# Kernel tuning notes

Measured on AMD Instinct MI355X. Metric: run time of the kernel, lower is better.

Reference implementation:

```python
import jax, jax.numpy as jnp
import numpy as np

B, SQ, QD = 8, 4096, 1280
SCTX, CD = 93, 2048
HEADS, DIM_HEAD = 20, 64
INNER = HEADS * DIM_HEAD  # 1280


def setup_inputs() -> dict:
    key = jax.random.key(0)
    ks = jax.random.split(key, 10)
    inp = {
        'x': jax.random.normal(ks[0], (B, SQ, QD), dtype=jnp.float32),
        'context': jax.random.normal(ks[1], (B, SCTX, CD), dtype=jnp.float32),
        'scale': jax.random.uniform(ks[2], (), dtype=jnp.float32),
        'num_img_token': 16,
        # learned parameters (PyTorch nn.Linear weight layout: [out, in])
        'Wq': jax.random.normal(ks[3], (INNER, QD), dtype=jnp.float32) * 0.02,
        'Wk': jax.random.normal(ks[4], (INNER, CD), dtype=jnp.float32) * 0.02,
        'Wv': jax.random.normal(ks[5], (INNER, CD), dtype=jnp.float32) * 0.02,
        'Wk_ip': jax.random.normal(ks[6], (INNER, CD), dtype=jnp.float32) * 0.02,
        'Wv_ip': jax.random.normal(ks[7], (INNER, CD), dtype=jnp.float32) * 0.02,
        'Wout': jax.random.normal(ks[8], (QD, INNER), dtype=jnp.float32) * 0.02,
        'b_out': jax.random.normal(ks[9], (QD,), dtype=jnp.float32) * 0.02,
    }
    return inp


def _heads(t):
    # [b, s, inner] -> [b, h, s, d]
    b, s, _ = t.shape
    return t.reshape(b, s, HEADS, DIM_HEAD).transpose(0, 2, 1, 3)


def _attn(q, k, v):
    # q: [b,h,sq,d], k/v: [b,h,skv,d]
    sm_scale = 1.0 / jnp.sqrt(jnp.asarray(DIM_HEAD, q.dtype))
    logits = jnp.einsum('bhqd,bhkd->bhqk', q, k) * sm_scale
    probs = jax.nn.softmax(logits, axis=-1)
    return jnp.einsum('bhqk,bhkd->bhqd', probs, v)


def reference(x, context, scale, num_img_token, Wq, Wk, Wv, Wk_ip, Wv_ip, Wout, b_out):
    eos = context.shape[1] - num_img_token
    txt_ctx = context[:, :eos, :]
    img_ctx = context[:, eos:, :]

    q = _heads(jnp.einsum('bsc,ic->bsi', x, Wq))
    k = _heads(jnp.einsum('bsc,ic->bsi', txt_ctx, Wk))
    v = _heads(jnp.einsum('bsc,ic->bsi', txt_ctx, Wv))
    k_i = _heads(jnp.einsum('bsc,ic->bsi', img_ctx, Wk_ip))
    v_i = _heads(jnp.einsum('bsc,ic->bsi', img_ctx, Wv_ip))

    txt_out = _attn(q, k, v)            # [b,h,sq,d]
    img_out = _attn(q, k_i, v_i)        # [b,h,sq,d]
    out = txt_out + scale * img_out

    out = out.transpose(0, 2, 1, 3).reshape(x.shape[0], x.shape[1], INNER)
    return jnp.einsum('bsi,oi->bso', out, Wout) + b_out
```

## Files before the change

### kernel.cpp

```cpp
#include <hip/hip_runtime.h>
#include <stdint.h>
#include <stddef.h>

typedef __attribute__((ext_vector_type(8))) short bf16x8;
typedef __attribute__((ext_vector_type(4))) short bf16x4;
typedef __attribute__((ext_vector_type(4))) float f32x4;

typedef const __attribute__((address_space(1))) uint32_t gas_u32;
typedef __attribute__((address_space(3))) uint32_t las_u32;

__device__ __forceinline__ short f2bf(float f) {
  union { float f; uint32_t u; } c; c.f = f;
  uint32_t u = c.u;
  u += 0x7fffu + ((u >> 16) & 1u);
  return (short)(u >> 16);
}

__global__ void k_cvt(const float* __restrict__ src, short* __restrict__ dst, int n) {
  int i = (blockIdx.x * 256 + threadIdx.x) * 4;
  if (i + 4 <= n) {
    float4 v = *(const float4*)(src + i);
    bf16x4 o = { f2bf(v.x), f2bf(v.y), f2bf(v.z), f2bf(v.w) };
    *(bf16x4*)(dst + i) = o;
  } else {
    for (; i < n; ++i) dst[i] = f2bf(src[i]);
  }
}

__global__ void k_cvt_ctx(const float* __restrict__ ctx, short* __restrict__ dst,
                          int rpb, int row0) {
  long total = 8L * rpb * 2048;
  long i = ((long)blockIdx.x * 256 + threadIdx.x) * 4;
  if (i >= total) return;
  int c = (int)(i & 2047);
  long rs = i >> 11;
  int b = (int)(rs / rpb);
  int s = (int)(rs - (long)b * rpb);
  const float* sp = ctx + ((long)(b * 93 + row0 + s) * 2048 + c);
  float4 v = *(const float4*)sp;
  bf16x4 o = { f2bf(v.x), f2bf(v.y), f2bf(v.z), f2bf(v.w) };
  *(bf16x4*)(dst + i) = o;
}

template <int MODE>
__global__ __launch_bounds__(256)
void k_gemm(const short* __restrict__ A, const short* __restrict__ Bm,
            void* __restrict__ out, const float* __restrict__ bias,
            int Mreal, int N, int K, int SPB) {
  __shared__ __align__(16) short As[128 * 32];
  __shared__ __align__(16) short Bs[128 * 32];
  const int t = threadIdx.x;
  const int lane = t & 63, wave = t >> 6;
  const int wm = (wave >> 1) * 64, wn = (wave & 1) * 64;
  const int m0 = blockIdx.y * 128, n0 = blockIdx.x * 128;
  const int q4 = lane >> 4, r16 = lane & 15;

  f32x4 zero = {0.f, 0.f, 0.f, 0.f};
  f32x4 acc[4][4];
#pragma unroll
  for (int i = 0; i < 4; ++i)
#pragma unroll
    for (int j = 0; j < 4; ++j) acc[i][j] = zero;

  const int p0 = t, p1 = t + 256;
  const int ar0 = p0 >> 2, ac0 = (((p0 & 3) ^ ((ar0 >> 1) & 3))) * 8;
  const int ar1 = p1 >> 2, ac1 = (((p1 & 3) ^ ((ar1 >> 1) & 3))) * 8;
  int gm0 = m0 + ar0; if (gm0 >= Mreal) gm0 = Mreal - 1;
  int gm1 = m0 + ar1; if (gm1 >= Mreal) gm1 = Mreal - 1;
  const short* ga0 = A + (size_t)gm0 * K + ac0;
  const short* ga1 = A + (size_t)gm1 * K + ac1;
  const short* gb0 = Bm + (size_t)(n0 + ar0) * K + ac0;
  const short* gb1 = Bm + (size_t)(n0 + ar1) * K + ac1;

  const int swz = (q4 ^ ((r16 >> 1) & 3)) * 8;

  for (int k0 = 0; k0 < K; k0 += 32) {
    __builtin_amdgcn_global_load_lds((gas_u32*)(ga0 + k0), (las_u32*)(As + p0 * 8), 16, 0, 0);
    __builtin_amdgcn_global_load_lds((gas_u32*)(ga1 + k0), (las_u32*)(As + p1 * 8), 16, 0, 0);
    __builtin_amdgcn_global_load_lds((gas_u32*)(gb0 + k0), (las_u32*)(Bs + p0 * 8), 16, 0, 0);
    __builtin_amdgcn_global_load_lds((gas_u32*)(gb1 + k0), (las_u32*)(Bs + p1 * 8), 16, 0, 0);
    __syncthreads();

    bf16x8 af[4], bf[4];
#pragma unroll
    for (int i = 0; i < 4; ++i)
      af[i] = *(const bf16x8*)(As + (wm + i * 16 + r16) * 32 + swz);
#pragma unroll
    for (int j = 0; j < 4; ++j)
      bf[j] = *(const bf16x8*)(Bs + (wn + j * 16 + r16) * 32 + swz);
#pragma unroll
    for (int i = 0; i < 4; ++i)
#pragma unroll
      for (int j = 0; j < 4; ++j)
        acc[i][j] = __builtin_amdgcn_mfma_f32_16x16x32_bf16(af[i], bf[j], acc[i][j], 0, 0, 0);
    __syncthreads();
  }

  if (MODE == 0) {
    short* O = (short*)out;
#pragma unroll
    for (int i = 0; i < 4; ++i) {
#pragma unroll
      for (int rr = 0; rr < 4; ++rr) {
        int m = m0 + wm + i * 16 + q4 * 4 + rr;
        if (m < Mreal) {
          int bb, ss;
          if (SPB == 4096) { bb = m >> 12; ss = m & 4095; }
          else             { bb = m / SPB; ss = m - bb * SPB; }
#pragma unroll
          for (int j = 0; j < 4; ++j) {
            int n = n0 + wn + j * 16 + r16;
            int h = n >> 6, d = n & 63;
            int grp = (h >= 20) ? 1 : 0;
            int hl = h - grp * 20;
            O[(((size_t)(grp * 160 + bb * 20 + hl)) * SPB + ss) * 64 + d] = f2bf(acc[i][j][rr]);
          }
        }
      }
    }
  } else {
    float* O = (float*)out;
#pragma unroll
    for (int i = 0; i < 4; ++i) {
#pragma unroll
      for (int rr = 0; rr < 4; ++rr) {
        int m = m0 + wm + i * 16 + q4 * 4 + rr;
        if (m < Mreal) {
#pragma unroll
          for (int j = 0; j < 4; ++j) {
            int n = n0 + wn + j * 16 + r16;
            O[(size_t)m * N + n] = acc[i][j][rr] + bias[n];
          }
        }
      }
    }
  }
}

__global__ __launch_bounds__(256)
void k_attn(const short* __restrict__ qb, const short* __restrict__ kb,
            const short* __restrict__ vb, const short* __restrict__ kib,
            const short* __restrict__ vib, const float* __restrict__ scale_p,
            short* __restrict__ out) {
  constexpr int KS = 72;
  constexpr int PS = 104;
  __shared__ __align__(16) short Ks[96 * KS];
  __shared__ __align__(16) short Vt[64 * PS];
  __shared__ __align__(16) short Pp[4][16 * PS];
  const int t = threadIdx.x, lane = t & 63, wave = t >> 6;
  const int q4 = lane >> 4, r16 = lane & 15;
  const int b = blockIdx.z, h = blockIdx.y, qt = blockIdx.x;
  const int bh = b * 20 + h;
  const short* kt = kb + (size_t)bh * 77 * 64;
  const short* vt = vb + (size_t)bh * 77 * 64;
  const short* ki = kib + (size_t)bh * 16 * 64;
  const short* vi = vib + (size_t)bh * 16 * 64;

  for (int c = t; c < 96 * 8; c += 256) {
    int row = c >> 3, o = (c & 7) * 8;
    uint4 val = {0u, 0u, 0u, 0u};
    if (row < 77)       val = *(const uint4*)(kt + row * 64 + o);
    else if (row >= 80) val = *(const uint4*)(ki + (row - 80) * 64 + o);
    *(uint4*)(Ks + row * KS + o) = val;
  }
  for (int i = t; i < 96 * 64; i += 256) {
    int key = i >> 6, d = i & 63;
    short v = 0;
    if (key < 77)       v = vt[key * 64 + d];
    else if (key >= 80) v = vi[(key - 80) * 64 + d];
    Vt[d * PS + key] = v;
  }
  __syncthreads();

  const int s0 = qt * 64 + wave * 16;
  const short* qp = qb + ((size_t)bh * 4096 + s0) * 64;
  bf16x8 qf[2];
#pragma unroll
  for (int kc = 0; kc < 2; ++kc)
    qf[kc] = *(const bf16x8*)(qp + r16 * 64 + kc * 32 + q4 * 8);

  f32x4 zero = {0.f, 0.f, 0.f, 0.f};
  f32x4 lg[6];
#pragma unroll
  for (int nt = 0; nt < 6; ++nt) {
    lg[nt] = zero;
#pragma unroll
    for (int kc = 0; kc < 2; ++kc) {
      bf16x8 kf = *(const bf16x8*)(Ks + (nt * 16 + r16) * KS + kc * 32 + q4 * 8);
      lg[nt] = __builtin_amdgcn_mfma_f32_16x16x32_bf16(qf[kc], kf, lg[nt], 0, 0, 0);
    }
  }

  const float sm = 0.125f;
  const float scl = scale_p[0];
#pragma unroll
  for (int nt = 0; nt < 6; ++nt)
#pragma unroll
    for (int rr = 0; rr < 4; ++rr) lg[nt][rr] *= sm;
  if (r16 >= 13) {
#pragma unroll
    for (int rr = 0; rr < 4; ++rr) lg[4][rr] = -1e30f;
  }

#pragma unroll
  for (int rr = 0; rr < 4; ++rr) {
    float mx = -1e30f;
#pragma unroll
    for (int nt = 0; nt < 5; ++nt) mx = fmaxf(mx, lg[nt][rr]);
#pragma unroll
    for (int o = 1; o < 16; o <<= 1) mx = fmaxf(mx, __shfl_xor(mx, o, 64));
    float s = 0.f;
#pragma unroll
    for (int nt = 0; nt < 5; ++nt) {
      float p = __expf(lg[nt][rr] - mx);
      lg[nt][rr] = p; s += p;
    }
#pragma unroll
    for (int o = 1; o < 16; o <<= 1) s += __shfl_xor(s, o, 64);
    float inv = 1.f / s;
#pragma unroll
    for (int nt = 0; nt < 5; ++nt) lg[nt][rr] *= inv;

    float mi = lg[5][rr];
#pragma unroll
    for (int o = 1; o < 16; o <<= 1) mi = fmaxf(mi, __shfl_xor(mi, o, 64));
    float pi = __expf(lg[5][rr] - mi);
    float si = pi;
#pragma unroll
    for (int o = 1; o < 16; o <<= 1) si += __shfl_xor(si, o, 64);
    lg[5][rr] = pi * (scl / si);
  }

  short* pw = &Pp[wave][0];
#pragma unroll
  for (int nt = 0; nt < 6; ++nt)
#pragma unroll
    for (int rr = 0; rr < 4; ++rr)
      pw[(q4 * 4 + rr) * PS + nt * 16 + r16] = f2bf(lg[nt][rr]);

  f32x4 oc[4];
#pragma unroll
  for (int dt = 0; dt < 4; ++dt) {
    oc[dt] = zero;
#pragma unroll
    for (int kc = 0; kc < 3; ++kc) {
      bf16x8 pf = *(const bf16x8*)(pw + r16 * PS + kc * 32 + q4 * 8);
      bf16x8 vf = *(const bf16x8*)(Vt + (dt * 16 + r16) * PS + kc * 32 + q4 * 8);
      oc[dt] = __builtin_amdgcn_mfma_f32_16x16x32_bf16(pf, vf, oc[dt], 0, 0, 0);
    }
  }

#pragma unroll
  for (int dt = 0; dt < 4; ++dt)
#pragma unroll
    for (int rr = 0; rr < 4; ++rr) {
      int m = s0 + q4 * 4 + rr;
      int d = dt * 16 + r16;
      out[((size_t)b * 4096 + m) * 1280 + h * 64 + d] = f2bf(oc[dt][rr]);
    }
}

extern "C" void kernel_launch(void* const* d_in, const int* in_sizes, int n_in,
                              void* d_out, int out_size, void* d_ws, size_t ws_size,
                              hipStream_t stream) {
  const float* x    = (const float*)d_in[0];
  const float* ctx  = (const float*)d_in[1];
  const float* scal = (const float*)d_in[2];
  const float* Wq   = (const float*)d_in[4];
  const float* Wk   = (const float*)d_in[5];
  const float* Wv   = (const float*)d_in[6];
  const float* Wkip = (const float*)d_in[7];
  const float* Wvip = (const float*)d_in[8];
  const float* Wout = (const float*)d_in[9];
  const float* bout = (const float*)d_in[10];
  float* out = (float*)d_out;

  char* ws = (char*)d_ws;
  size_t off = 0;
  auto alloc = [&](size_t elems) -> short* {
    short* p = (short*)(ws + off);
    off += (elems * 2 + 255) & ~(size_t)255;
    return p;
  };
  short* xb    = alloc(32768UL * 1280);
  short* txtb  = alloc(616UL * 2048);
  short* imgb  = alloc(128UL * 2048);
  short* Wqb   = alloc(1280UL * 1280);
  short* Wkvb  = alloc(2UL * 1280 * 2048);
  short* Wkvip = alloc(2UL * 1280 * 2048);
  short* Woutb = alloc(1280UL * 1280);
  short* qb    = alloc(32768UL * 1280);
  short* kb    = alloc(2UL * 160 * 77 * 64);
  short* kib   = alloc(2UL * 160 * 16 * 64);
  short* vb    = kb  + 160UL * 77 * 64;
  short* vib   = kib + 160UL * 16 * 64;
  short* attnb = xb;

  auto cvt = [&](const float* s, short* d, long n) {
    int blocks = (int)((n / 4 + 255) / 256);
    k_cvt<<<blocks, 256, 0, stream>>>(s, d, (int)n);
  };
  cvt(x, xb, 32768L * 1280);
  cvt(Wq, Wqb, 1280L * 1280);
  cvt(Wk,   Wkvb,                 1280L * 2048);
  cvt(Wv,   Wkvb + 1280L * 2048,  1280L * 2048);
  cvt(Wkip, Wkvip,                1280L * 2048);
  cvt(Wvip, Wkvip + 1280L * 2048, 1280L * 2048);
  cvt(Wout, Woutb, 1280L * 1280);
  {
    long n1 = 8L * 77 * 2048;
    k_cvt_ctx<<<(int)((n1 / 4 + 255) / 256), 256, 0, stream>>>(ctx, txtb, 77, 0);
    long n2 = 8L * 16 * 2048;
    k_cvt_ctx<<<(int)((n2 / 4 + 255) / 256), 256, 0, stream>>>(ctx, imgb, 16, 77);
  }

  { dim3 g(10, 256); k_gemm<0><<<g, 256, 0, stream>>>(xb, Wqb, qb, nullptr, 32768, 1280, 1280, 4096); }
  { dim3 g(20, 5);
    k_gemm<0><<<g, 256, 0, stream>>>(txtb, Wkvb, kb, nullptr, 616, 2560, 2048, 77); }
  { dim3 g(20, 1);
    k_gemm<0><<<g, 256, 0, stream>>>(imgb, Wkvip, kib, nullptr, 128, 2560, 2048, 16); }
  { dim3 g(64, 20, 8);
    k_attn<<<g, 256, 0, stream>>>(qb, kb, vb, kib, vib, scal, attnb); }
  { dim3 g(10, 256);
    k_gemm<1><<<g, 256, 0, stream>>>(attnb, Woutb, out, bout, 32768, 1280, 1280, 1); }
}
```

Measured before the change: 884.0 us.

## Double-buffer GEMM LDS tiles and remap workgroups across XCDs

The GEMM main loop now ping-pongs between two LDS buffers. The global-to-LDS load for the next K slice is issued while MFMAs run on the current slice, which halves the barriers per step and hides load latency. Workgroup IDs are also remapped so that consecutive tiles land on the same XCD, aiming for better L2 reuse. LDS use doubles, and the loop assumes K is a multiple of 64 for its prologue/epilogue structure.

```diff
diff --git a/kernel.cpp b/kernel.cpp
--- a/kernel.cpp
+++ b/kernel.cpp
@@ -42,17 +42,54 @@
   *(bf16x4*)(dst + i) = o;
 }
 
+struct GFrag { bf16x8 a[4]; bf16x8 b[4]; };
+
+__device__ __forceinline__ void g_ld(GFrag& f, const short* as, const short* bs,
+                                     int wm, int wn, int r16, int swz) {
+#pragma unroll
+  for (int i = 0; i < 4; ++i)
+    f.a[i] = *(const bf16x8*)(as + (wm + i * 16 + r16) * 32 + swz);
+#pragma unroll
+  for (int j = 0; j < 4; ++j)
+    f.b[j] = *(const bf16x8*)(bs + (wn + j * 16 + r16) * 32 + swz);
+}
+
+__device__ __forceinline__ void g_mm(const GFrag& f, f32x4 acc[4][4]) {
+#pragma unroll
+  for (int i = 0; i < 4; ++i)
+#pragma unroll
+    for (int j = 0; j < 4; ++j)
+      acc[i][j] = __builtin_amdgcn_mfma_f32_16x16x32_bf16(f.a[i], f.b[j], acc[i][j], 0, 0, 0);
+}
+
+__device__ __forceinline__ void g_stage(short* asd, short* bsd,
+                                        const short* ga0, const short* ga1,
+                                        const short* gb0, const short* gb1,
+                                        int k0, int p0, int p1) {
+  __builtin_amdgcn_global_load_lds((gas_u32*)(ga0 + k0), (las_u32*)(asd + p0 * 8), 16, 0, 0);
+  __builtin_amdgcn_global_load_lds((gas_u32*)(ga1 + k0), (las_u32*)(asd + p1 * 8), 16, 0, 0);
+  __builtin_amdgcn_global_load_lds((gas_u32*)(gb0 + k0), (las_u32*)(bsd + p0 * 8), 16, 0, 0);
+  __builtin_amdgcn_global_load_lds((gas_u32*)(gb1 + k0), (las_u32*)(bsd + p1 * 8), 16, 0, 0);
+}
+
 template <int MODE>
 __global__ __launch_bounds__(256)
 void k_gemm(const short* __restrict__ A, const short* __restrict__ Bm,
             void* __restrict__ out, const float* __restrict__ bias,
             int Mreal, int N, int K, int SPB) {
-  __shared__ __align__(16) short As[128 * 32];
-  __shared__ __align__(16) short Bs[128 * 32];
+  __shared__ __align__(16) short As[2][128 * 32];
+  __shared__ __align__(16) short Bs[2][128 * 32];
   const int t = threadIdx.x;
   const int lane = t & 63, wave = t >> 6;
   const int wm = (wave >> 1) * 64, wn = (wave & 1) * 64;
-  const int m0 = blockIdx.y * 128, n0 = blockIdx.x * 128;
+
+  const int nwg = gridDim.x * gridDim.y;
+  const int lin = blockIdx.y * gridDim.x + blockIdx.x;
+  const int qq = nwg >> 3, r8 = nwg & 7;
+  const int xcd = lin & 7, idx = lin >> 3;
+  const int wg = (xcd < r8 ? xcd * (qq + 1) : r8 * (qq + 1) + (xcd - r8) * qq) + idx;
+  const int bx = wg % gridDim.x, by = wg / gridDim.x;
+  const int m0 = by * 128, n0 = bx * 128;
   const int q4 = lane >> 4, r16 = lane & 15;
 
   f32x4 zero = {0.f, 0.f, 0.f, 0.f};
@@ -74,27 +111,27 @@
 
   const int swz = (q4 ^ ((r16 >> 1) & 3)) * 8;
 
-  for (int k0 = 0; k0 < K; k0 += 32) {
-    __builtin_amdgcn_global_load_lds((gas_u32*)(ga0 + k0), (las_u32*)(As + p0 * 8), 16, 0, 0);
-    __builtin_amdgcn_global_load_lds((gas_u32*)(ga1 + k0), (las_u32*)(As + p1 * 8), 16, 0, 0);
-    __builtin_amdgcn_global_load_lds((gas_u32*)(gb0 + k0), (las_u32*)(Bs + p0 * 8), 16, 0, 0);
-    __builtin_amdgcn_global_load_lds((gas_u32*)(gb1 + k0), (las_u32*)(Bs + p1 * 8), 16, 0, 0);
+  g_stage(&As[0][0], &Bs[0][0], ga0, ga1, gb0, gb1, 0, p0, p1);
+  __syncthreads();
+
+  GFrag f;
+  for (int k0 = 32; k0 < K - 32; k0 += 64) {
+    g_ld(f, &As[0][0], &Bs[0][0], wm, wn, r16, swz);
+    g_stage(&As[1][0], &Bs[1][0], ga0, ga1, gb0, gb1, k0, p0, p1);
+    g_mm(f, acc);
     __syncthreads();
 
-    bf16x8 af[4], bf[4];
-#pragma unroll
-    for (int i = 0; i < 4; ++i)
-      af[i] = *(const bf16x8*)(As + (wm + i * 16 + r16) * 32 + swz);
-#pragma unroll
-    for (int j = 0; j < 4; ++j)
-      bf[j] = *(const bf16x8*)(Bs + (wn + j * 16 + r16) * 32 + swz);
-#pragma unroll
-    for (int i = 0; i < 4; ++i)
-#pragma unroll
-      for (int j = 0; j < 4; ++j)
-        acc[i][j] = __builtin_amdgcn_mfma_f32_16x16x32_bf16(af[i], bf[j], acc[i][j], 0, 0, 0);
+    g_ld(f, &As[1][0], &Bs[1][0], wm, wn, r16, swz);
+    g_stage(&As[0][0], &Bs[0][0], ga0, ga1, gb0, gb1, k0 + 32, p0, p1);
+    g_mm(f, acc);
     __syncthreads();
   }
+  g_ld(f, &As[0][0], &Bs[0][0], wm, wn, r16, swz);
+  g_stage(&As[1][0], &Bs[1][0], ga0, ga1, gb0, gb1, K - 32, p0, p1);
+  g_mm(f, acc);
+  __syncthreads();
+  g_ld(f, &As[1][0], &Bs[1][0], wm, wn, r16, swz);
+  g_mm(f, acc);
 
   if (MODE == 0) {
     short* O = (short*)out;
```

Result: faster. 823.1 us (-6.9%).
